# Performance work log

Measured on AMD Instinct MI355X. Metric: run time of the kernel, lower is better.

Reference implementation:

```python
import jax, jax.numpy as jnp
import numpy as np

B, C = 20000, 8          # trees, children (leaves) per tree
WORD, TAG, MEM = 300, 50, 150


def gru_cell(x, h, w_ih, w_hh, b_ih, b_hh):
    # torch.nn.GRUCell math; gate order r, z, n
    gi = x @ w_ih.T + b_ih
    gh = h @ w_hh.T + b_hh
    ir, iz, i_n = jnp.split(gi, 3, axis=-1)
    hr, hz, hn = jnp.split(gh, 3, axis=-1)
    r = jax.nn.sigmoid(ir + hr)
    z = jax.nn.sigmoid(iz + hz)
    n = jnp.tanh(i_n + r * hn)
    return (1.0 - z) * n + z * h


def setup_inputs() -> dict:
    key = jax.random.key(0)
    ks = jax.random.split(key, 16)
    s = 0.05  # small init scale for weights
    return {
        "embs": jax.random.normal(ks[0], (B, C, WORD), jnp.float32),
        "tags": jax.random.normal(ks[1], (B, C, TAG), jnp.float32),
        "tag_parent": jax.random.normal(ks[2], (B, TAG), jnp.float32),
        "w_ih_leaf": jax.random.normal(ks[3], (3 * MEM, WORD + TAG), jnp.float32) * s,
        "w_hh_leaf": jax.random.normal(ks[4], (3 * MEM, MEM), jnp.float32) * s,
        "b_ih_leaf": jax.random.normal(ks[5], (3 * MEM,), jnp.float32) * s,
        "b_hh_leaf": jax.random.normal(ks[6], (3 * MEM,), jnp.float32) * s,
        "w_ih_child": jax.random.normal(ks[7], (3 * MEM, MEM + 2 * TAG), jnp.float32) * s,
        "w_hh_child": jax.random.normal(ks[8], (3 * MEM, MEM), jnp.float32) * s,
        "b_ih_child": jax.random.normal(ks[9], (3 * MEM,), jnp.float32) * s,
        "b_hh_child": jax.random.normal(ks[10], (3 * MEM,), jnp.float32) * s,
        "w_ih_node": jax.random.normal(ks[11], (3 * MEM, 1), jnp.float32) * s,
        "w_hh_node": jax.random.normal(ks[12], (3 * MEM, MEM), jnp.float32) * s,
        "b_ih_node": jax.random.normal(ks[13], (3 * MEM,), jnp.float32) * s,
        "b_hh_node": jax.random.normal(ks[14], (3 * MEM,), jnp.float32) * s,
    }


def reference(embs, tags, tag_parent,
              w_ih_leaf, w_hh_leaf, b_ih_leaf, b_hh_leaf,
              w_ih_child, w_hh_child, b_ih_child, b_hh_child,
              w_ih_node, w_hh_node, b_ih_node, b_hh_node):
    # 1) all leaves at once: GRUCell(concat(word, tag), h=0)  -> [B, C, MEM]
    x_leaf = jnp.concatenate([embs, tags], axis=-1)            # [B, C, WORD+TAG]
    h0 = jnp.zeros((B, C, MEM), x_leaf.dtype)
    leaf_h = gru_cell(x_leaf, h0, w_ih_leaf, w_hh_leaf, b_ih_leaf, b_hh_leaf)

    # 2) child inputs: concat(child state, child tag, parent tag)  -> [B, C, MEM+2*TAG]
    tp = jnp.broadcast_to(tag_parent[:, None, :], (B, C, TAG))
    x_child = jnp.concatenate([leaf_h, tags, tp], axis=-1)

    # 3) sequential left-to-right fold over children with children GRUCell
    def step(h, x_i):
        h_new = gru_cell(x_i, h, w_ih_child, w_hh_child, b_ih_child, b_hh_child)
        return h_new, None

    h_init = jnp.zeros((B, MEM), x_leaf.dtype)
    h_final, _ = jax.lax.scan(step, h_init, jnp.swapaxes(x_child, 0, 1))  # scan over C

    # 4) node GRUCell with x = zeros(1)
    x_zeros = jnp.zeros((B, 1), x_leaf.dtype)
    root = gru_cell(x_zeros, h_final, w_ih_node, w_hh_node, b_ih_node, b_hh_node)
    return root  # [B, MEM]
```

## Files before the change

### kernel.cpp

```cpp
#include <hip/hip_runtime.h>


typedef _Float16 f16;
typedef _Float16 f16x4 __attribute__((ext_vector_type(4)));
typedef _Float16 f16x8 __attribute__((ext_vector_type(8)));
typedef float f32x4 __attribute__((ext_vector_type(4)));

namespace {

constexpr int NTREE = 20000;
constexpr int CCH   = 8;
constexpr int WORD  = 300;
constexpr int TAGD  = 50;
constexpr int MEMD  = 150;
constexpr int NBLK  = 250;

constexpr int KT_L = 11;
constexpr int KT_I = 8;
constexpr int KT_H = 5;
constexpr int KT_N = 5;
constexpr int NTILE = 30;

constexpr size_t OFF_WL   = 0;
constexpr size_t OFF_WI   = OFF_WL + (size_t)KT_L * NTILE * 64 * 16;
constexpr size_t OFF_WH   = OFF_WI + (size_t)KT_I * NTILE * 64 * 16;
constexpr size_t OFF_WN   = OFF_WH + (size_t)KT_H * NTILE * 64 * 16;
constexpr size_t OFF_BIAS = OFF_WN + (size_t)KT_N * NTILE * 64 * 16;
constexpr size_t OFF_DATA = OFF_BIAS + 16 * 160 * 4;

constexpr size_t GI_BYTES = (size_t)CCH * NBLK * 15 * 640 * 8;
constexpr size_t WS_R3    = OFF_DATA + GI_BYTES;
constexpr int    HW_S  = 152;
constexpr size_t WS_R2 = OFF_DATA + (size_t)CCH * NTREE * HW_S * 2;


__device__ __forceinline__ float sigmoid_f(float x) {
  return 1.0f / (1.0f + __expf(-x));
}
__device__ __forceinline__ float tanh_f(float x) {
  float ax = fabsf(x);
  float e  = __expf(-2.0f * ax);
  float t  = (1.0f - e) / (1.0f + e);
  return copysignf(t, x);
}

__global__ void prep_kernel(const float* __restrict__ w_ih_leaf,
                            const float* __restrict__ b_ih_leaf,
                            const float* __restrict__ b_hh_leaf,
                            const float* __restrict__ w_ih_child,
                            const float* __restrict__ w_hh_child,
                            const float* __restrict__ b_ih_child,
                            const float* __restrict__ b_hh_child,
                            const float* __restrict__ w_hh_node,
                            const float* __restrict__ b_ih_node,
                            const float* __restrict__ b_hh_node,
                            char* __restrict__ ws) {
  const int NWL = KT_L * NTILE * 64;
  const int NWI = KT_I * NTILE * 64;
  const int NWH = KT_H * NTILE * 64;
  const int NWN = KT_N * NTILE * 64;
  int t = blockIdx.x * blockDim.x + threadIdx.x;

  if (t < NWL) {
    int kt = t / (NTILE * 64), rem = t % (NTILE * 64);
    int nt = rem / 64, l = rem % 64;
    int gate = nt / 10, jt = nt % 10;
    int j = jt * 16 + (l & 15);
    bool valid = j < MEMD;
    int g = gate * MEMD + (valid ? j : 0);
    f16x8 v;
#pragma unroll
    for (int e = 0; e < 8; ++e) {
      int k = kt * 32 + ((l >> 4) * 8) + e;
      v[e] = (f16)((valid && k < WORD + TAGD) ? w_ih_leaf[g * (WORD + TAGD) + k] : 0.0f);
    }
    ((f16x8*)(ws + OFF_WL))[t] = v;
    return;
  }
  t -= NWL;
  if (t < NWI) {
    int kt = t / (NTILE * 64), rem = t % (NTILE * 64);
    int nt = rem / 64, l = rem % 64;
    int gate = nt / 10, jt = nt % 10;
    int j = jt * 16 + (l & 15);
    bool valid = j < MEMD;
    int g = gate * MEMD + (valid ? j : 0);
    f16x8 v;
#pragma unroll
    for (int e = 0; e < 8; ++e) {
      int k = kt * 32 + ((l >> 4) * 8) + e;
      int src = (k < 150) ? k : (k >= 152 && k < 252) ? (k - 2) : -1;
      v[e] = (f16)((valid && src >= 0) ? w_ih_child[g * 250 + src] : 0.0f);
    }
    ((f16x8*)(ws + OFF_WI))[t] = v;
    return;
  }
  t -= NWI;
  if (t < NWH) {
    int kt = t / (NTILE * 64), rem = t % (NTILE * 64);
    int nt = rem / 64, l = rem % 64;
    int gate = nt / 10, jt = nt % 10;
    int j = jt * 16 + (l & 15);
    bool valid = j < MEMD;
    int g = gate * MEMD + (valid ? j : 0);
    f16x8 v;
#pragma unroll
    for (int e = 0; e < 8; ++e) {
      int k = kt * 32 + ((l >> 4) * 8) + e;
      v[e] = (f16)((valid && k < MEMD) ? w_hh_child[g * MEMD + k] : 0.0f);
    }
    ((f16x8*)(ws + OFF_WH))[t] = v;
    return;
  }
  t -= NWH;
  if (t < NWN) {
    int kt = t / (NTILE * 64), rem = t % (NTILE * 64);
    int nt = rem / 64, l = rem % 64;
    int gate = nt / 10, jt = nt % 10;
    int j = jt * 16 + (l & 15);
    bool valid = j < MEMD;
    int g = gate * MEMD + (valid ? j : 0);
    f16x8 v;
#pragma unroll
    for (int e = 0; e < 8; ++e) {
      int k = kt * 32 + ((l >> 4) * 8) + e;
      v[e] = (f16)((valid && k < MEMD) ? w_hh_node[g * MEMD + k] : 0.0f);
    }
    ((f16x8*)(ws + OFF_WN))[t] = v;
    return;
  }
  t -= NWN;
  if (t < 16 * 160) {
    int arr = t / 160, j = t % 160;
    float v = 0.0f;
    if (j < MEMD) {
      switch (arr) {
        case 0:  v = b_ih_leaf[j] + b_hh_leaf[j]; break;
        case 1:  v = b_ih_leaf[MEMD + j] + b_hh_leaf[MEMD + j]; break;
        case 2:  v = b_ih_leaf[2 * MEMD + j]; break;
        case 3:  v = b_hh_leaf[2 * MEMD + j]; break;
        case 4:  v = b_ih_child[j] + b_hh_child[j]; break;
        case 5:  v = b_ih_child[MEMD + j] + b_hh_child[MEMD + j]; break;
        case 6:  v = b_ih_child[2 * MEMD + j]; break;
        case 7:  v = b_hh_child[2 * MEMD + j]; break;
        case 8:  v = b_ih_node[j] + b_hh_node[j]; break;
        case 9:  v = b_ih_node[MEMD + j] + b_hh_node[MEMD + j]; break;
        case 10: v = b_ih_node[2 * MEMD + j]; break;
        case 11: v = b_hh_node[2 * MEMD + j]; break;
        case 12: v = b_ih_child[j]; break;
        case 13: v = b_ih_child[MEMD + j]; break;
        case 14: v = b_hh_child[j]; break;
        case 15: v = b_hh_child[MEMD + j]; break;
      }
    }
    ((float*)(ws + OFF_BIAS))[arr * 160 + j] = v;
  }
}

__global__ __launch_bounds__(640, 2)
void leaf3_kernel(const float* __restrict__ embs,
                  const float* __restrict__ tags,
                  const float* __restrict__ tag_parent,
                  char* __restrict__ ws) {
  extern __shared__ char lsm[];
  f16* xle = (f16*)lsm;
  f16* xch = xle + 80 * 360;

  const f16x8* WL   = (const f16x8*)(ws + OFF_WL);
  const f16x8* WI   = (const f16x8*)(ws + OFF_WI);
  const float* BIAS = (const float*)(ws + OFF_BIAS);

  const int tid = threadIdx.x, lane = tid & 63, w = tid >> 6;
  const int blk = blockIdx.x, c = blockIdx.y, t0 = blk * 80;
  const int arow = lane & 15, acol8 = (lane >> 4) * 8, qrow = (lane >> 4) * 4;
  const int j = w * 16 + arow;
  const bool jok = j < MEMD;

  for (int i = tid; i < 80 * 150; i += 640) {
    int r = i / 150, k2 = i - r * 150;
    float2 v = *(const float2*)(embs + ((size_t)(t0 + r) * CCH + c) * WORD + 2 * k2);
    xle[r * 360 + 2 * k2]     = (f16)v.x;
    xle[r * 360 + 2 * k2 + 1] = (f16)v.y;
  }
  for (int i = tid; i < 80 * 25; i += 640) {
    int r = i / 25, k2 = i - r * 25;
    float2 v = *(const float2*)(tags + ((size_t)(t0 + r) * CCH + c) * TAGD + 2 * k2);
    xle[r * 360 + 300 + 2 * k2]     = (f16)v.x;
    xle[r * 360 + 300 + 2 * k2 + 1] = (f16)v.y;
  }
  for (int i = tid; i < 80 * 25; i += 640) {
    int r = i / 25, k2 = i - r * 25;
    float2 v = *(const float2*)(tag_parent + (size_t)(t0 + r) * TAGD + 2 * k2);
    xch[r * 264 + 202 + 2 * k2] = (f16)v.x;
    xch[r * 264 + 203 + 2 * k2] = (f16)v.y;
  }
  for (int i = tid; i < 80 * 14; i += 640) {
    int r = i / 14, k = i - r * 14;
    int col = (k < 2) ? (150 + k) : (250 + k);
    xch[r * 264 + col] = (f16)0.0f;
  }
  for (int i = tid; i < 80; i += 640) {
    xle[i * 360 + 350] = (f16)0.0f;
    xle[i * 360 + 351] = (f16)0.0f;
  }
  __syncthreads();

  for (int i = tid; i < 80 * 50; i += 640) {
    int r = i / 50, tt = i - r * 50;
    xch[r * 264 + 152 + tt] = xle[r * 360 + 300 + tt];
  }

  f32x4 aR[5], aZ[5], aN[5];
#pragma unroll
  for (int m = 0; m < 5; ++m) { aR[m] = 0.f; aZ[m] = 0.f; aN[m] = 0.f; }
  for (int kt = 0; kt < KT_L; ++kt) {
    f16x8 br = WL[(kt * NTILE + w) * 64 + lane];
    f16x8 bz = WL[(kt * NTILE + 10 + w) * 64 + lane];
    f16x8 bn = WL[(kt * NTILE + 20 + w) * 64 + lane];
    const f16* ab = xle + kt * 32 + acol8;
#pragma unroll
    for (int m = 0; m < 5; ++m) {
      f16x8 a = *(const f16x8*)(ab + (16 * m + arow) * 360);
      aR[m] = __builtin_amdgcn_mfma_f32_16x16x32_f16(a, br, aR[m], 0, 0, 0);
      aZ[m] = __builtin_amdgcn_mfma_f32_16x16x32_f16(a, bz, aZ[m], 0, 0, 0);
      aN[m] = __builtin_amdgcn_mfma_f32_16x16x32_f16(a, bn, aN[m], 0, 0, 0);
    }
  }

  {
    const float bLr = BIAS[j], bLz = BIAS[160 + j], bLi = BIAS[320 + j], bLh = BIAS[480 + j];
#pragma unroll
    for (int m = 0; m < 5; ++m) {
#pragma unroll
      for (int q = 0; q < 4; ++q) {
        float rg = sigmoid_f(aR[m][q] + bLr);
        float zg = sigmoid_f(aZ[m][q] + bLz);
        float ng = tanh_f(aN[m][q] + bLi + rg * bLh);
        float h  = (1.0f - zg) * ng;
        if (jok) xch[(16 * m + qrow + q) * 264 + j] = (f16)h;
      }
    }
  }
  __syncthreads();

  f32x4 cR[5], cZ[5], cN[5];
#pragma unroll
  for (int m = 0; m < 5; ++m) { cR[m] = 0.f; cZ[m] = 0.f; cN[m] = 0.f; }
  for (int kt = 0; kt < KT_I; ++kt) {
    f16x8 br = WI[(kt * NTILE + w) * 64 + lane];
    f16x8 bz = WI[(kt * NTILE + 10 + w) * 64 + lane];
    f16x8 bn = WI[(kt * NTILE + 20 + w) * 64 + lane];
    const f16* ab = xch + kt * 32 + acol8;
#pragma unroll
    for (int m = 0; m < 5; ++m) {
      f16x8 a = *(const f16x8*)(ab + (16 * m + arow) * 264);
      cR[m] = __builtin_amdgcn_mfma_f32_16x16x32_f16(a, br, cR[m], 0, 0, 0);
      cZ[m] = __builtin_amdgcn_mfma_f32_16x16x32_f16(a, bz, cZ[m], 0, 0, 0);
      cN[m] = __builtin_amdgcn_mfma_f32_16x16x32_f16(a, bn, cN[m], 0, 0, 0);
    }
  }

  {
    const float bir = BIAS[12 * 160 + j], biz = BIAS[13 * 160 + j], bin = BIAS[6 * 160 + j];
    char* gib = ws + OFF_DATA + ((((size_t)c * NBLK + blk) * 15) * 640 + tid) * 8;
#pragma unroll
    for (int m = 0; m < 5; ++m) {
      f16x4 vr, vz, vn;
#pragma unroll
      for (int q = 0; q < 4; ++q) {
        vr[q] = (f16)(cR[m][q] + bir);
        vz[q] = (f16)(cZ[m][q] + biz);
        vn[q] = (f16)(cN[m][q] + bin);
      }
      *(f16x4*)(gib + (size_t)(m * 3 + 0) * 640 * 8) = vr;
      *(f16x4*)(gib + (size_t)(m * 3 + 1) * 640 * 8) = vz;
      *(f16x4*)(gib + (size_t)(m * 3 + 2) * 640 * 8) = vn;
    }
  }
}

__global__ __launch_bounds__(640, 2)
void fold3_kernel(const char* __restrict__ ws,
                  float* __restrict__ out) {
  __shared__ f16 hls[80 * 168];

  const f16x8* WH   = (const f16x8*)(ws + OFF_WH);
  const f16x8* WN   = (const f16x8*)(ws + OFF_WN);
  const float* BIAS = (const float*)(ws + OFF_BIAS);

  const int tid = threadIdx.x, lane = tid & 63, w = tid >> 6;
  const int blk = blockIdx.x, t0 = blk * 80;
  const int arow = lane & 15, acol8 = (lane >> 4) * 8, qrow = (lane >> 4) * 4;
  const int j = w * 16 + arow;
  const bool jok = j < MEMD;

  const float bhr = BIAS[14 * 160 + j], bhz = BIAS[15 * 160 + j], bhn = BIAS[7 * 160 + j];
  const float bNr = BIAS[8 * 160 + j],  bNz = BIAS[9 * 160 + j];
  const float bNi = BIAS[10 * 160 + j], bNh = BIAS[11 * 160 + j];

  for (int i = tid; i < 1680; i += 640) ((int4*)hls)[i] = make_int4(0, 0, 0, 0);
  __syncthreads();

  const char* gib = ws + OFF_DATA + ((size_t)blk * 15 * 640 + tid) * 8;
  constexpr size_t CSTRIDE = (size_t)NBLK * 15 * 640 * 8;

  f16x4 gbuf[2][15];
#pragma unroll
  for (int u = 0; u < 15; ++u)
    gbuf[0][u] = *(const f16x4*)(gib + (size_t)u * 640 * 8);

  f32x4 hp[5];
#pragma unroll
  for (int m = 0; m < 5; ++m) hp[m] = 0.f;

#pragma unroll
  for (int c = 0; c < CCH; ++c) {
    if (c < CCH - 1) {
#pragma unroll
      for (int u = 0; u < 15; ++u)
        gbuf[(c + 1) & 1][u] =
            *(const f16x4*)(gib + (size_t)(c + 1) * CSTRIDE + (size_t)u * 640 * 8);
    }

    f32x4 aR[5], aZ[5], aNh[5];
#pragma unroll
    for (int m = 0; m < 5; ++m) { aR[m] = 0.f; aZ[m] = 0.f; aNh[m] = 0.f; }
    for (int kt = 0; kt < KT_H; ++kt) {
      f16x8 br = WH[(kt * NTILE + w) * 64 + lane];
      f16x8 bz = WH[(kt * NTILE + 10 + w) * 64 + lane];
      f16x8 bn = WH[(kt * NTILE + 20 + w) * 64 + lane];
      const f16* ab = hls + kt * 32 + acol8;
#pragma unroll
      for (int m = 0; m < 5; ++m) {
        f16x8 a = *(const f16x8*)(ab + (16 * m + arow) * 168);
        aR[m]  = __builtin_amdgcn_mfma_f32_16x16x32_f16(a, br, aR[m], 0, 0, 0);
        aZ[m]  = __builtin_amdgcn_mfma_f32_16x16x32_f16(a, bz, aZ[m], 0, 0, 0);
        aNh[m] = __builtin_amdgcn_mfma_f32_16x16x32_f16(a, bn, aNh[m], 0, 0, 0);
      }
    }
    __syncthreads();

#pragma unroll
    for (int m = 0; m < 5; ++m) {
#pragma unroll
      for (int q = 0; q < 4; ++q) {
        int row = 16 * m + qrow + q;
        float gr = (float)gbuf[c & 1][m * 3 + 0][q];
        float gz = (float)gbuf[c & 1][m * 3 + 1][q];
        float gn = (float)gbuf[c & 1][m * 3 + 2][q];
        float rg = sigmoid_f(gr + aR[m][q] + bhr);
        float zg = sigmoid_f(gz + aZ[m][q] + bhz);
        float ng = tanh_f(gn + rg * (aNh[m][q] + bhn));
        float h  = (1.0f - zg) * ng + zg * hp[m][q];
        hp[m][q] = h;
        if (jok) hls[row * 168 + j] = (f16)h;
      }
    }
    __syncthreads();
  }

  f32x4 aR[5], aZ[5], aNh[5];
#pragma unroll
  for (int m = 0; m < 5; ++m) { aR[m] = 0.f; aZ[m] = 0.f; aNh[m] = 0.f; }
  for (int kt = 0; kt < KT_N; ++kt) {
    f16x8 br = WN[(kt * NTILE + w) * 64 + lane];
    f16x8 bz = WN[(kt * NTILE + 10 + w) * 64 + lane];
    f16x8 bn = WN[(kt * NTILE + 20 + w) * 64 + lane];
    const f16* ab = hls + kt * 32 + acol8;
#pragma unroll
    for (int m = 0; m < 5; ++m) {
      f16x8 a = *(const f16x8*)(ab + (16 * m + arow) * 168);
      aR[m]  = __builtin_amdgcn_mfma_f32_16x16x32_f16(a, br, aR[m], 0, 0, 0);
      aZ[m]  = __builtin_amdgcn_mfma_f32_16x16x32_f16(a, bz, aZ[m], 0, 0, 0);
      aNh[m] = __builtin_amdgcn_mfma_f32_16x16x32_f16(a, bn, aNh[m], 0, 0, 0);
    }
  }
#pragma unroll
  for (int m = 0; m < 5; ++m) {
#pragma unroll
    for (int q = 0; q < 4; ++q) {
      int row = 16 * m + qrow + q;
      float rg = sigmoid_f(aR[m][q] + bNr);
      float zg = sigmoid_f(aZ[m][q] + bNz);
      float ng = tanh_f(bNi + rg * (aNh[m][q] + bNh));
      float o  = (1.0f - zg) * ng + zg * hp[m][q];
      if (jok) out[(size_t)(t0 + row) * MEMD + j] = o;
    }
  }
}

namespace r2 {

__global__ __launch_bounds__(640)
void leaf_kernel(const float* __restrict__ embs,
                 const float* __restrict__ tags,
                 char* __restrict__ ws) {
  __shared__ f16 xle[80 * 360];
  const f16x8* WL   = (const f16x8*)(ws + OFF_WL);
  const float* BIAS = (const float*)(ws + OFF_BIAS);
  f16* hws = (f16*)(ws + OFF_DATA);

  const int tid = threadIdx.x, lane = tid & 63, w = tid >> 6;
  const int c = blockIdx.y, t0 = blockIdx.x * 80;
  const int arow = lane & 15, acol8 = (lane >> 4) * 8, qrow = (lane >> 4) * 4;
  const int j = w * 16 + (lane & 15);

  for (int i = tid; i < 80 * 150; i += 640) {
    int r = i / 150, k2 = i - r * 150;
    float2 v = *(const float2*)(embs + ((size_t)(t0 + r) * CCH + c) * WORD + 2 * k2);
    xle[r * 360 + 2 * k2]     = (f16)v.x;
    xle[r * 360 + 2 * k2 + 1] = (f16)v.y;
  }
  for (int i = tid; i < 80 * 25; i += 640) {
    int r = i / 25, k2 = i - r * 25;
    float2 v = *(const float2*)(tags + ((size_t)(t0 + r) * CCH + c) * TAGD + 2 * k2);
    xle[r * 360 + 300 + 2 * k2]     = (f16)v.x;
    xle[r * 360 + 300 + 2 * k2 + 1] = (f16)v.y;
  }
  for (int i = tid; i < 80; i += 640) {
    xle[i * 360 + 350] = (f16)0.0f;
    xle[i * 360 + 351] = (f16)0.0f;
  }
  __syncthreads();

  f32x4 aR[5], aZ[5], aN[5];
#pragma unroll
  for (int m = 0; m < 5; ++m) { aR[m] = 0.f; aZ[m] = 0.f; aN[m] = 0.f; }
  for (int kt = 0; kt < KT_L; ++kt) {
    f16x8 br = WL[(kt * NTILE + w) * 64 + lane];
    f16x8 bz = WL[(kt * NTILE + 10 + w) * 64 + lane];
    f16x8 bn = WL[(kt * NTILE + 20 + w) * 64 + lane];
    const f16* ab = xle + kt * 32 + acol8;
#pragma unroll
    for (int m = 0; m < 5; ++m) {
      f16x8 a = *(const f16x8*)(ab + (16 * m + arow) * 360);
      aR[m] = __builtin_amdgcn_mfma_f32_16x16x32_f16(a, br, aR[m], 0, 0, 0);
      aZ[m] = __builtin_amdgcn_mfma_f32_16x16x32_f16(a, bz, aZ[m], 0, 0, 0);
      aN[m] = __builtin_amdgcn_mfma_f32_16x16x32_f16(a, bn, aN[m], 0, 0, 0);
    }
  }
  const float bLr = BIAS[j], bLz = BIAS[160 + j], bLi = BIAS[320 + j], bLh = BIAS[480 + j];
#pragma unroll
  for (int m = 0; m < 5; ++m) {
#pragma unroll
    for (int q = 0; q < 4; ++q) {
      int row = 16 * m + qrow + q;
      float rg = sigmoid_f(aR[m][q] + bLr);
      float zg = sigmoid_f(aZ[m][q] + bLz);
      float ng = tanh_f(aN[m][q] + bLi + rg * bLh);
      float h  = (1.0f - zg) * ng;
      if (j < HW_S)
        hws[((size_t)c * NTREE + t0 + row) * HW_S + j] = (f16)(j < MEMD ? h : 0.0f);
    }
  }
}

__global__ __launch_bounds__(640)
void fold_kernel(const float* __restrict__ tags,
                 const float* __restrict__ tag_parent,
                 const char* __restrict__ ws,
                 float* __restrict__ out) {
  extern __shared__ char fsm[];
  f16* xch0 = (f16*)fsm;
  f16* xch1 = xch0 + 80 * 264;
  f16* hls  = xch1 + 80 * 264;

  const f16x8* WI   = (const f16x8*)(ws + OFF_WI);
  const f16x8* WH   = (const f16x8*)(ws + OFF_WH);
  const f16x8* WN   = (const f16x8*)(ws + OFF_WN);
  const float* BIAS = (const float*)(ws + OFF_BIAS);
  const f16*   hws  = (const f16*)(ws + OFF_DATA);

  const int tid = threadIdx.x, lane = tid & 63, w = tid >> 6;
  const int t0 = blockIdx.x * 80;
  const int arow = lane & 15, acol8 = (lane >> 4) * 8, qrow = (lane >> 4) * 4;
  const int j = w * 16 + (lane & 15);
  const bool jok = j < MEMD;

  const float bCr = BIAS[4 * 160 + j], bCz = BIAS[5 * 160 + j];
  const float bCi = BIAS[6 * 160 + j], bCh = BIAS[7 * 160 + j];
  const float bNr = BIAS[8 * 160 + j], bNz = BIAS[9 * 160 + j];
  const float bNi = BIAS[10 * 160 + j], bNh = BIAS[11 * 160 + j];

  for (int i = tid; i < 1680; i += 640) ((int4*)hls)[i] = make_int4(0, 0, 0, 0);
  for (int i = tid; i < 80 * 25; i += 640) {
    int r = i / 25, k2 = i - r * 25;
    float2 v = *(const float2*)(tag_parent + (size_t)(t0 + r) * TAGD + 2 * k2);
    f16 a = (f16)v.x, b = (f16)v.y;
    xch0[r * 264 + 202 + 2 * k2] = a; xch0[r * 264 + 203 + 2 * k2] = b;
    xch1[r * 264 + 202 + 2 * k2] = a; xch1[r * 264 + 203 + 2 * k2] = b;
  }
  for (int i = tid; i < 80 * 4; i += 640) {
    int r = i >> 2, k = i & 3;
    xch0[r * 264 + 252 + k] = (f16)0.0f;
    xch1[r * 264 + 252 + k] = (f16)0.0f;
  }
#pragma unroll
  for (int s = 0; s < 3; ++s) {
    int i = tid + 640 * s;
    if (i < 1520) {
      int r = i / 19, q = i - r * 19;
      *(f16x8*)(xch0 + r * 264 + 8 * q) =
          *(const f16x8*)(hws + ((size_t)(t0 + r)) * HW_S + 8 * q);
    }
  }
#pragma unroll
  for (int s = 0; s < 4; ++s) {
    int i = tid + 640 * s;
    if (i < 2000) {
      int r = i / 25, k2 = i - r * 25;
      float2 v = *(const float2*)(tags + ((size_t)(t0 + r) * CCH) * TAGD + 2 * k2);
      xch0[r * 264 + 152 + 2 * k2] = (f16)v.x;
      xch0[r * 264 + 153 + 2 * k2] = (f16)v.y;
    }
  }
  __syncthreads();

  f32x4 hp[5];
#pragma unroll
  for (int m = 0; m < 5; ++m) hp[m] = 0.f;

  f16* xc = xch0;
  f16* xa = xch1;

  for (int c = 0; c < CCH; ++c) {
    f16x8 ph[3];
    float2 pt[4];
    if (c < 7) {
#pragma unroll
      for (int s = 0; s < 3; ++s) {
        int i = tid + 640 * s;
        if (i < 1520) {
          int r = i / 19, q = i - r * 19;
          ph[s] = *(const f16x8*)(hws + ((size_t)(c + 1) * NTREE + t0 + r) * HW_S + 8 * q);
        }
      }
#pragma unroll
      for (int s = 0; s < 4; ++s) {
        int i = tid + 640 * s;
        if (i < 2000) {
          int r = i / 25, k2 = i - r * 25;
          pt[s] = *(const float2*)(tags + ((size_t)(t0 + r) * CCH + (c + 1)) * TAGD + 2 * k2);
        }
      }
    }

    f32x4 aR[5], aZ[5], aNi[5], aNh[5];
#pragma unroll
    for (int m = 0; m < 5; ++m) { aR[m] = 0.f; aZ[m] = 0.f; aNi[m] = 0.f; aNh[m] = 0.f; }
    for (int kt = 0; kt < KT_I; ++kt) {
      f16x8 br = WI[(kt * NTILE + w) * 64 + lane];
      f16x8 bz = WI[(kt * NTILE + 10 + w) * 64 + lane];
      f16x8 bn = WI[(kt * NTILE + 20 + w) * 64 + lane];
      const f16* ab = xc + kt * 32 + acol8;
#pragma unroll
      for (int m = 0; m < 5; ++m) {
        f16x8 a = *(const f16x8*)(ab + (16 * m + arow) * 264);
        aR[m]  = __builtin_amdgcn_mfma_f32_16x16x32_f16(a, br, aR[m], 0, 0, 0);
        aZ[m]  = __builtin_amdgcn_mfma_f32_16x16x32_f16(a, bz, aZ[m], 0, 0, 0);
        aNi[m] = __builtin_amdgcn_mfma_f32_16x16x32_f16(a, bn, aNi[m], 0, 0, 0);
      }
    }
    for (int kt = 0; kt < KT_H; ++kt) {
      f16x8 br = WH[(kt * NTILE + w) * 64 + lane];
      f16x8 bz = WH[(kt * NTILE + 10 + w) * 64 + lane];
      f16x8 bn = WH[(kt * NTILE + 20 + w) * 64 + lane];
      const f16* ab = hls + kt * 32 + acol8;
#pragma unroll
      for (int m = 0; m < 5; ++m) {
        f16x8 a = *(const f16x8*)(ab + (16 * m + arow) * 168);
        aR[m]  = __builtin_amdgcn_mfma_f32_16x16x32_f16(a, br, aR[m], 0, 0, 0);
        aZ[m]  = __builtin_amdgcn_mfma_f32_16x16x32_f16(a, bz, aZ[m], 0, 0, 0);
        aNh[m] = __builtin_amdgcn_mfma_f32_16x16x32_f16(a, bn, aNh[m], 0, 0, 0);
      }
    }
    __syncthreads();

    if (c < 7) {
#pragma unroll
      for (int s = 0; s < 3; ++s) {
        int i = tid + 640 * s;
        if (i < 1520) {
          int r = i / 19, q = i - r * 19;
          *(f16x8*)(xa + r * 264 + 8 * q) = ph[s];
        }
      }
#pragma unroll
      for (int s = 0; s < 4; ++s) {
        int i = tid + 640 * s;
        if (i < 2000) {
          int r = i / 25, k2 = i - r * 25;
          xa[r * 264 + 152 + 2 * k2] = (f16)pt[s].x;
          xa[r * 264 + 153 + 2 * k2] = (f16)pt[s].y;
        }
      }
    }

#pragma unroll
    for (int m = 0; m < 5; ++m) {
#pragma unroll
      for (int q = 0; q < 4; ++q) {
        int row = 16 * m + qrow + q;
        float rg = sigmoid_f(aR[m][q] + bCr);
        float zg = sigmoid_f(aZ[m][q] + bCz);
        float ng = tanh_f(aNi[m][q] + bCi + rg * (aNh[m][q] + bCh));
        float h  = (1.0f - zg) * ng + zg * hp[m][q];
        hp[m][q] = h;
        if (jok) hls[row * 168 + j] = (f16)h;
      }
    }
    __syncthreads();
    f16* tsw = xc; xc = xa; xa = tsw;
  }

  f32x4 aR[5], aZ[5], aNh[5];
#pragma unroll
  for (int m = 0; m < 5; ++m) { aR[m] = 0.f; aZ[m] = 0.f; aNh[m] = 0.f; }
  for (int kt = 0; kt < KT_N; ++kt) {
    f16x8 br = WN[(kt * NTILE + w) * 64 + lane];
    f16x8 bz = WN[(kt * NTILE + 10 + w) * 64 + lane];
    f16x8 bn = WN[(kt * NTILE + 20 + w) * 64 + lane];
    const f16* ab = hls + kt * 32 + acol8;
#pragma unroll
    for (int m = 0; m < 5; ++m) {
      f16x8 a = *(const f16x8*)(ab + (16 * m + arow) * 168);
      aR[m]  = __builtin_amdgcn_mfma_f32_16x16x32_f16(a, br, aR[m], 0, 0, 0);
      aZ[m]  = __builtin_amdgcn_mfma_f32_16x16x32_f16(a, bz, aZ[m], 0, 0, 0);
      aNh[m] = __builtin_amdgcn_mfma_f32_16x16x32_f16(a, bn, aNh[m], 0, 0, 0);
    }
  }
#pragma unroll
  for (int m = 0; m < 5; ++m) {
#pragma unroll
    for (int q = 0; q < 4; ++q) {
      int row = 16 * m + qrow + q;
      float rg = sigmoid_f(aR[m][q] + bNr);
      float zg = sigmoid_f(aZ[m][q] + bNz);
      float ng = tanh_f(bNi + rg * (aNh[m][q] + bNh));
      float o  = (1.0f - zg) * ng + zg * hp[m][q];
      if (jok) out[(size_t)(t0 + row) * MEMD + j] = o;
    }
  }
}

}

}

extern "C" void kernel_launch(void* const* d_in, const int* in_sizes, int n_in,
                              void* d_out, int out_size, void* d_ws, size_t ws_size,
                              hipStream_t stream) {
  const float* embs       = (const float*)d_in[0];
  const float* tags       = (const float*)d_in[1];
  const float* tag_parent = (const float*)d_in[2];
  const float* w_ih_leaf  = (const float*)d_in[3];
  const float* b_ih_leaf  = (const float*)d_in[5];
  const float* b_hh_leaf  = (const float*)d_in[6];
  const float* w_ih_child = (const float*)d_in[7];
  const float* w_hh_child = (const float*)d_in[8];
  const float* b_ih_child = (const float*)d_in[9];
  const float* b_hh_child = (const float*)d_in[10];
  const float* w_hh_node  = (const float*)d_in[12];
  const float* b_ih_node  = (const float*)d_in[13];
  const float* b_hh_node  = (const float*)d_in[14];
  float* out = (float*)d_out;
  char*  ws  = (char*)d_ws;

  prep_kernel<<<228, 256, 0, stream>>>(w_ih_leaf, b_ih_leaf, b_hh_leaf,
                                       w_ih_child, w_hh_child, b_ih_child, b_hh_child,
                                       w_hh_node, b_ih_node, b_hh_node, ws);

  if (ws_size >= WS_R3) {
    constexpr int LEAF_LDS = (80 * 360 + 80 * 264) * 2;
    hipFuncSetAttribute((const void*)leaf3_kernel,
                        hipFuncAttributeMaxDynamicSharedMemorySize, LEAF_LDS);
    leaf3_kernel<<<dim3(NBLK, CCH), 640, LEAF_LDS, stream>>>(embs, tags, tag_parent, ws);
    fold3_kernel<<<NBLK, 640, 0, stream>>>(ws, out);
  } else {
    r2::leaf_kernel<<<dim3(NBLK, CCH), 640, 0, stream>>>(embs, tags, ws);
    constexpr int FOLD_LDS = (2 * 80 * 264 + 80 * 168) * 2;
    hipFuncSetAttribute((const void*)r2::fold_kernel,
                        hipFuncAttributeMaxDynamicSharedMemorySize, FOLD_LDS);
    r2::fold_kernel<<<NBLK, 640, FOLD_LDS, stream>>>(tags, tag_parent, ws, out);
  }
}
```

Before: 448.3 us.

## Retile leaf kernel to 32-tree blocks and restructure fold gate-input layout

The leaf kernel now processes 32 trees per 320-thread block (625×8 grid) using static LDS, with each wave computing two output column tiles. This aims for higher occupancy and better load balance across CUs. The gate-input buffer is re-laid out per 16-row tile group so the fold kernel reads coalesced chunks. The fold kernel now keeps the r-gate weights in registers and skips the hidden matmul at step 0, where the hidden state is zero. It also drops the double-buffered prefetch in favour of per-step loads and raises its occupancy hint, which may expose global latency.

```diff
diff --git a/kernel.cpp b/kernel.cpp
--- a/kernel.cpp
+++ b/kernel.cpp
@@ -14,6 +14,7 @@
 constexpr int TAGD  = 50;
 constexpr int MEMD  = 150;
 constexpr int NBLK  = 250;
+constexpr int LBLK  = 625;
 
 constexpr int KT_L = 11;
 constexpr int KT_I = 8;
@@ -28,7 +29,9 @@
 constexpr size_t OFF_BIAS = OFF_WN + (size_t)KT_N * NTILE * 64 * 16;
 constexpr size_t OFF_DATA = OFF_BIAS + 16 * 160 * 4;
 
-constexpr size_t GI_BYTES = (size_t)CCH * NBLK * 15 * 640 * 8;
+constexpr size_t TG_BYTES = 15360;
+constexpr size_t C_STRIDE = (size_t)1250 * TG_BYTES;
+constexpr size_t GI_BYTES = (size_t)CCH * C_STRIDE;
 constexpr size_t WS_R3    = OFF_DATA + GI_BYTES;
 constexpr int    HW_S  = 152;
 constexpr size_t WS_R2 = OFF_DATA + (size_t)CCH * NTREE * HW_S * 2;
@@ -157,129 +160,146 @@
   }
 }
 
-__global__ __launch_bounds__(640, 2)
+__global__ __launch_bounds__(320, 5)
 void leaf3_kernel(const float* __restrict__ embs,
                   const float* __restrict__ tags,
                   const float* __restrict__ tag_parent,
                   char* __restrict__ ws) {
-  extern __shared__ char lsm[];
-  f16* xle = (f16*)lsm;
-  f16* xch = xle + 80 * 360;
+  __shared__ f16 xle[32 * 360];
+  __shared__ f16 xch[32 * 264];
 
   const f16x8* WL   = (const f16x8*)(ws + OFF_WL);
   const f16x8* WI   = (const f16x8*)(ws + OFF_WI);
   const float* BIAS = (const float*)(ws + OFF_BIAS);
 
   const int tid = threadIdx.x, lane = tid & 63, w = tid >> 6;
-  const int blk = blockIdx.x, c = blockIdx.y, t0 = blk * 80;
+  const int blk = blockIdx.x, c = blockIdx.y, t0 = blk * 32;
   const int arow = lane & 15, acol8 = (lane >> 4) * 8, qrow = (lane >> 4) * 4;
-  const int j = w * 16 + arow;
-  const bool jok = j < MEMD;
-
-  for (int i = tid; i < 80 * 150; i += 640) {
-    int r = i / 150, k2 = i - r * 150;
-    float2 v = *(const float2*)(embs + ((size_t)(t0 + r) * CCH + c) * WORD + 2 * k2);
-    xle[r * 360 + 2 * k2]     = (f16)v.x;
-    xle[r * 360 + 2 * k2 + 1] = (f16)v.y;
-  }
-  for (int i = tid; i < 80 * 25; i += 640) {
+  const int jt0 = 2 * w, jt1 = 2 * w + 1;
+  const int j0 = jt0 * 16 + arow;
+  const int j1 = jt1 * 16 + arow;
+  const bool j1ok = j1 < MEMD;
+
+  for (int i = tid; i < 32 * 75; i += 320) {
+    int r = i / 75, k4 = i - r * 75;
+    float4 v = *(const float4*)(embs + ((size_t)(t0 + r) * CCH + c) * WORD + 4 * k4);
+    f16* p = xle + r * 360 + 4 * k4;
+    p[0] = (f16)v.x; p[1] = (f16)v.y; p[2] = (f16)v.z; p[3] = (f16)v.w;
+  }
+  for (int i = tid; i < 32 * 25; i += 320) {
     int r = i / 25, k2 = i - r * 25;
     float2 v = *(const float2*)(tags + ((size_t)(t0 + r) * CCH + c) * TAGD + 2 * k2);
     xle[r * 360 + 300 + 2 * k2]     = (f16)v.x;
     xle[r * 360 + 300 + 2 * k2 + 1] = (f16)v.y;
   }
-  for (int i = tid; i < 80 * 25; i += 640) {
+  for (int i = tid; i < 32 * 25; i += 320) {
     int r = i / 25, k2 = i - r * 25;
     float2 v = *(const float2*)(tag_parent + (size_t)(t0 + r) * TAGD + 2 * k2);
     xch[r * 264 + 202 + 2 * k2] = (f16)v.x;
     xch[r * 264 + 203 + 2 * k2] = (f16)v.y;
   }
-  for (int i = tid; i < 80 * 14; i += 640) {
-    int r = i / 14, k = i - r * 14;
+  for (int i = tid; i < 32 * 6; i += 320) {
+    int r = i / 6, k = i - r * 6;
     int col = (k < 2) ? (150 + k) : (250 + k);
     xch[r * 264 + col] = (f16)0.0f;
   }
-  for (int i = tid; i < 80; i += 640) {
+  for (int i = tid; i < 32; i += 320) {
     xle[i * 360 + 350] = (f16)0.0f;
     xle[i * 360 + 351] = (f16)0.0f;
   }
   __syncthreads();
 
-  for (int i = tid; i < 80 * 50; i += 640) {
+  for (int i = tid; i < 32 * 50; i += 320) {
     int r = i / 50, tt = i - r * 50;
     xch[r * 264 + 152 + tt] = xle[r * 360 + 300 + tt];
   }
 
-  f32x4 aR[5], aZ[5], aN[5];
-#pragma unroll
-  for (int m = 0; m < 5; ++m) { aR[m] = 0.f; aZ[m] = 0.f; aN[m] = 0.f; }
+  f32x4 acc[2][3][2];
+#pragma unroll
+  for (int a = 0; a < 2; ++a)
+#pragma unroll
+    for (int g = 0; g < 3; ++g)
+#pragma unroll
+      for (int m = 0; m < 2; ++m) acc[a][g][m] = 0.f;
+
   for (int kt = 0; kt < KT_L; ++kt) {
-    f16x8 br = WL[(kt * NTILE + w) * 64 + lane];
-    f16x8 bz = WL[(kt * NTILE + 10 + w) * 64 + lane];
-    f16x8 bn = WL[(kt * NTILE + 20 + w) * 64 + lane];
-    const f16* ab = xle + kt * 32 + acol8;
-#pragma unroll
-    for (int m = 0; m < 5; ++m) {
-      f16x8 a = *(const f16x8*)(ab + (16 * m + arow) * 360);
-      aR[m] = __builtin_amdgcn_mfma_f32_16x16x32_f16(a, br, aR[m], 0, 0, 0);
-      aZ[m] = __builtin_amdgcn_mfma_f32_16x16x32_f16(a, bz, aZ[m], 0, 0, 0);
-      aN[m] = __builtin_amdgcn_mfma_f32_16x16x32_f16(a, bn, aN[m], 0, 0, 0);
-    }
+    f16x8 a0 = *(const f16x8*)(xle + kt * 32 + acol8 + (arow)      * 360);
+    f16x8 a1 = *(const f16x8*)(xle + kt * 32 + acol8 + (16 + arow) * 360);
+#pragma unroll
+    for (int jtp = 0; jtp < 2; ++jtp)
+#pragma unroll
+      for (int g = 0; g < 3; ++g) {
+        f16x8 b = WL[(kt * NTILE + g * 10 + 2 * w + jtp) * 64 + lane];
+        acc[jtp][g][0] = __builtin_amdgcn_mfma_f32_16x16x32_f16(a0, b, acc[jtp][g][0], 0, 0, 0);
+        acc[jtp][g][1] = __builtin_amdgcn_mfma_f32_16x16x32_f16(a1, b, acc[jtp][g][1], 0, 0, 0);
+      }
   }
 
   {
-    const float bLr = BIAS[j], bLz = BIAS[160 + j], bLi = BIAS[320 + j], bLh = BIAS[480 + j];
-#pragma unroll
-    for (int m = 0; m < 5; ++m) {
+    float bLr0 = BIAS[j0],       bLr1 = BIAS[j1];
+    float bLz0 = BIAS[160 + j0], bLz1 = BIAS[160 + j1];
+    float bLi0 = BIAS[320 + j0], bLi1 = BIAS[320 + j1];
+    float bLh0 = BIAS[480 + j0], bLh1 = BIAS[480 + j1];
+#pragma unroll
+    for (int m = 0; m < 2; ++m)
 #pragma unroll
       for (int q = 0; q < 4; ++q) {
-        float rg = sigmoid_f(aR[m][q] + bLr);
-        float zg = sigmoid_f(aZ[m][q] + bLz);
-        float ng = tanh_f(aN[m][q] + bLi + rg * bLh);
-        float h  = (1.0f - zg) * ng;
-        if (jok) xch[(16 * m + qrow + q) * 264 + j] = (f16)h;
-      }
-    }
+        int row = 16 * m + qrow + q;
+        float rg0 = sigmoid_f(acc[0][0][m][q] + bLr0);
+        float zg0 = sigmoid_f(acc[0][1][m][q] + bLz0);
+        float ng0 = tanh_f(acc[0][2][m][q] + bLi0 + rg0 * bLh0);
+        xch[row * 264 + j0] = (f16)((1.0f - zg0) * ng0);
+        float rg1 = sigmoid_f(acc[1][0][m][q] + bLr1);
+        float zg1 = sigmoid_f(acc[1][1][m][q] + bLz1);
+        float ng1 = tanh_f(acc[1][2][m][q] + bLi1 + rg1 * bLh1);
+        if (j1ok) xch[row * 264 + j1] = (f16)((1.0f - zg1) * ng1);
+      }
   }
   __syncthreads();
 
-  f32x4 cR[5], cZ[5], cN[5];
-#pragma unroll
-  for (int m = 0; m < 5; ++m) { cR[m] = 0.f; cZ[m] = 0.f; cN[m] = 0.f; }
+#pragma unroll
+  for (int a = 0; a < 2; ++a)
+#pragma unroll
+    for (int g = 0; g < 3; ++g)
+#pragma unroll
+      for (int m = 0; m < 2; ++m) acc[a][g][m] = 0.f;
+
   for (int kt = 0; kt < KT_I; ++kt) {
-    f16x8 br = WI[(kt * NTILE + w) * 64 + lane];
-    f16x8 bz = WI[(kt * NTILE + 10 + w) * 64 + lane];
-    f16x8 bn = WI[(kt * NTILE + 20 + w) * 64 + lane];
-    const f16* ab = xch + kt * 32 + acol8;
-#pragma unroll
-    for (int m = 0; m < 5; ++m) {
-      f16x8 a = *(const f16x8*)(ab + (16 * m + arow) * 264);
-      cR[m] = __builtin_amdgcn_mfma_f32_16x16x32_f16(a, br, cR[m], 0, 0, 0);
-      cZ[m] = __builtin_amdgcn_mfma_f32_16x16x32_f16(a, bz, cZ[m], 0, 0, 0);
-      cN[m] = __builtin_amdgcn_mfma_f32_16x16x32_f16(a, bn, cN[m], 0, 0, 0);
-    }
+    f16x8 a0 = *(const f16x8*)(xch + kt * 32 + acol8 + (arow)      * 264);
+    f16x8 a1 = *(const f16x8*)(xch + kt * 32 + acol8 + (16 + arow) * 264);
+#pragma unroll
+    for (int jtp = 0; jtp < 2; ++jtp)
+#pragma unroll
+      for (int g = 0; g < 3; ++g) {
+        f16x8 b = WI[(kt * NTILE + g * 10 + 2 * w + jtp) * 64 + lane];
+        acc[jtp][g][0] = __builtin_amdgcn_mfma_f32_16x16x32_f16(a0, b, acc[jtp][g][0], 0, 0, 0);
+        acc[jtp][g][1] = __builtin_amdgcn_mfma_f32_16x16x32_f16(a1, b, acc[jtp][g][1], 0, 0, 0);
+      }
   }
 
   {
-    const float bir = BIAS[12 * 160 + j], biz = BIAS[13 * 160 + j], bin = BIAS[6 * 160 + j];
-    char* gib = ws + OFF_DATA + ((((size_t)c * NBLK + blk) * 15) * 640 + tid) * 8;
-#pragma unroll
-    for (int m = 0; m < 5; ++m) {
-      f16x4 vr, vz, vn;
-#pragma unroll
-      for (int q = 0; q < 4; ++q) {
-        vr[q] = (f16)(cR[m][q] + bir);
-        vz[q] = (f16)(cZ[m][q] + biz);
-        vn[q] = (f16)(cN[m][q] + bin);
-      }
-      *(f16x4*)(gib + (size_t)(m * 3 + 0) * 640 * 8) = vr;
-      *(f16x4*)(gib + (size_t)(m * 3 + 1) * 640 * 8) = vz;
-      *(f16x4*)(gib + (size_t)(m * 3 + 2) * 640 * 8) = vn;
-    }
-  }
-}
-
-__global__ __launch_bounds__(640, 2)
+    float bi0[3] = {BIAS[12 * 160 + j0], BIAS[13 * 160 + j0], BIAS[6 * 160 + j0]};
+    float bi1[3] = {BIAS[12 * 160 + j1], BIAS[13 * 160 + j1], BIAS[6 * 160 + j1]};
+#pragma unroll
+    for (int m = 0; m < 2; ++m) {
+      int tg = blk * 2 + m;
+      char* base = ws + OFF_DATA + (size_t)c * C_STRIDE + (size_t)tg * TG_BYTES + (size_t)lane * 8;
+#pragma unroll
+      for (int g = 0; g < 3; ++g) {
+        f16x4 v0, v1;
+#pragma unroll
+        for (int q = 0; q < 4; ++q) {
+          v0[q] = (f16)(acc[0][g][m][q] + bi0[g]);
+          v1[q] = (f16)(acc[1][g][m][q] + bi1[g]);
+        }
+        *(f16x4*)(base + (size_t)(g * 10 + jt0) * 512) = v0;
+        *(f16x4*)(base + (size_t)(g * 10 + jt1) * 512) = v1;
+      }
+    }
+  }
+}
+
+__global__ __launch_bounds__(640, 3)
 void fold3_kernel(const char* __restrict__ ws,
                   float* __restrict__ out) {
   __shared__ f16 hls[80 * 168];
@@ -298,16 +318,17 @@
   const float bNr = BIAS[8 * 160 + j],  bNz = BIAS[9 * 160 + j];
   const float bNi = BIAS[10 * 160 + j], bNh = BIAS[11 * 160 + j];
 
-  for (int i = tid; i < 1680; i += 640) ((int4*)hls)[i] = make_int4(0, 0, 0, 0);
-  __syncthreads();
-
-  const char* gib = ws + OFF_DATA + ((size_t)blk * 15 * 640 + tid) * 8;
-  constexpr size_t CSTRIDE = (size_t)NBLK * 15 * 640 * 8;
-
-  f16x4 gbuf[2][15];
-#pragma unroll
-  for (int u = 0; u < 15; ++u)
-    gbuf[0][u] = *(const f16x4*)(gib + (size_t)u * 640 * 8);
+  for (int i = tid; i < 80 * 18; i += 640) {
+    int r = i / 18;
+    hls[r * 168 + 150 + (i - r * 18)] = (f16)0.0f;
+  }
+
+  f16x8 whr[5];
+#pragma unroll
+  for (int kt = 0; kt < KT_H; ++kt) whr[kt] = WH[(kt * NTILE + w) * 64 + lane];
+
+  const char* gbase = ws + OFF_DATA + (size_t)(blk * 5) * TG_BYTES +
+                      (size_t)w * 512 + (size_t)lane * 8;
 
   f32x4 hp[5];
 #pragma unroll
@@ -315,47 +336,46 @@
 
 #pragma unroll
   for (int c = 0; c < CCH; ++c) {
-    if (c < CCH - 1) {
-#pragma unroll
-      for (int u = 0; u < 15; ++u)
-        gbuf[(c + 1) & 1][u] =
-            *(const f16x4*)(gib + (size_t)(c + 1) * CSTRIDE + (size_t)u * 640 * 8);
-    }
+    f16x4 gbuf[15];
+#pragma unroll
+    for (int m = 0; m < 5; ++m)
+#pragma unroll
+      for (int g = 0; g < 3; ++g)
+        gbuf[m * 3 + g] = *(const f16x4*)(gbase + (size_t)c * C_STRIDE +
+                                          (size_t)m * TG_BYTES + (size_t)g * 5120);
 
     f32x4 aR[5], aZ[5], aNh[5];
 #pragma unroll
     for (int m = 0; m < 5; ++m) { aR[m] = 0.f; aZ[m] = 0.f; aNh[m] = 0.f; }
-    for (int kt = 0; kt < KT_H; ++kt) {
-      f16x8 br = WH[(kt * NTILE + w) * 64 + lane];
-      f16x8 bz = WH[(kt * NTILE + 10 + w) * 64 + lane];
-      f16x8 bn = WH[(kt * NTILE + 20 + w) * 64 + lane];
-      const f16* ab = hls + kt * 32 + acol8;
-#pragma unroll
-      for (int m = 0; m < 5; ++m) {
-        f16x8 a = *(const f16x8*)(ab + (16 * m + arow) * 168);
-        aR[m]  = __builtin_amdgcn_mfma_f32_16x16x32_f16(a, br, aR[m], 0, 0, 0);
-        aZ[m]  = __builtin_amdgcn_mfma_f32_16x16x32_f16(a, bz, aZ[m], 0, 0, 0);
-        aNh[m] = __builtin_amdgcn_mfma_f32_16x16x32_f16(a, bn, aNh[m], 0, 0, 0);
-      }
-    }
-    __syncthreads();
-
-#pragma unroll
-    for (int m = 0; m < 5; ++m) {
+
+    if (c != 0) {
+      for (int kt = 0; kt < KT_H; ++kt) {
+        f16x8 bz = WH[(kt * NTILE + 10 + w) * 64 + lane];
+        f16x8 bn = WH[(kt * NTILE + 20 + w) * 64 + lane];
+        const f16* ab = hls + kt * 32 + acol8;
+#pragma unroll
+        for (int m = 0; m < 5; ++m) {
+          f16x8 a = *(const f16x8*)(ab + (16 * m + arow) * 168);
+          aR[m]  = __builtin_amdgcn_mfma_f32_16x16x32_f16(a, whr[kt], aR[m], 0, 0, 0);
+          aZ[m]  = __builtin_amdgcn_mfma_f32_16x16x32_f16(a, bz, aZ[m], 0, 0, 0);
+          aNh[m] = __builtin_amdgcn_mfma_f32_16x16x32_f16(a, bn, aNh[m], 0, 0, 0);
+        }
+      }
+      __syncthreads();
+    }
+
+#pragma unroll
+    for (int m = 0; m < 5; ++m)
 #pragma unroll
       for (int q = 0; q < 4; ++q) {
         int row = 16 * m + qrow + q;
-        float gr = (float)gbuf[c & 1][m * 3 + 0][q];
-        float gz = (float)gbuf[c & 1][m * 3 + 1][q];
-        float gn = (float)gbuf[c & 1][m * 3 + 2][q];
-        float rg = sigmoid_f(gr + aR[m][q] + bhr);
-        float zg = sigmoid_f(gz + aZ[m][q] + bhz);
-        float ng = tanh_f(gn + rg * (aNh[m][q] + bhn));
+        float rg = sigmoid_f((float)gbuf[m * 3 + 0][q] + aR[m][q] + bhr);
+        float zg = sigmoid_f((float)gbuf[m * 3 + 1][q] + aZ[m][q] + bhz);
+        float ng = tanh_f((float)gbuf[m * 3 + 2][q] + rg * (aNh[m][q] + bhn));
         float h  = (1.0f - zg) * ng + zg * hp[m][q];
         hp[m][q] = h;
         if (jok) hls[row * 168 + j] = (f16)h;
       }
-    }
     __syncthreads();
   }
 
@@ -376,7 +396,7 @@
     }
   }
 #pragma unroll
-  for (int m = 0; m < 5; ++m) {
+  for (int m = 0; m < 5; ++m)
 #pragma unroll
     for (int q = 0; q < 4; ++q) {
       int row = 16 * m + qrow + q;
@@ -386,7 +406,6 @@
       float o  = (1.0f - zg) * ng + zg * hp[m][q];
       if (jok) out[(size_t)(t0 + row) * MEMD + j] = o;
     }
-  }
 }
 
 namespace r2 {
@@ -671,10 +690,7 @@
                                        w_hh_node, b_ih_node, b_hh_node, ws);
 
   if (ws_size >= WS_R3) {
-    constexpr int LEAF_LDS = (80 * 360 + 80 * 264) * 2;
-    hipFuncSetAttribute((const void*)leaf3_kernel,
-                        hipFuncAttributeMaxDynamicSharedMemorySize, LEAF_LDS);
-    leaf3_kernel<<<dim3(NBLK, CCH), 640, LEAF_LDS, stream>>>(embs, tags, tag_parent, ws);
+    leaf3_kernel<<<dim3(LBLK, CCH), 320, 0, stream>>>(embs, tags, tag_parent, ws);
     fold3_kernel<<<NBLK, 640, 0, stream>>>(ws, out);
   } else {
     r2::leaf_kernel<<<dim3(NBLK, CCH), 640, 0, stream>>>(embs, tags, ws);
```

New measurement: 537.0 us. 1.2x slower.
